# Optimization experiments

Measured on AMD Instinct MI355X. Metric: run time of the kernel, lower is better.

Reference implementation:

```python
import jax, jax.numpy as jnp
import numpy as np

TOPK = 10
MIN_SIM = 0.8
MIN_VOTES = 0.0
REMOVE_INNER_THR = 0.8
NUM_CLASSES = 1000
D, C, N = 256, 256, 500000


def setup_inputs() -> dict:
    key = jax.random.key(0)
    k1, k2, k3, k4, k5 = jax.random.split(key, 5)
    # query descriptors, L2-normalized (cosine similarity, matches min_sim=0.8 semantics)
    q = jax.random.normal(k1, (D, C), dtype=jnp.float32)
    q = q / jnp.linalg.norm(q, axis=1, keepdims=True)
    # database descriptors + integer place_id stored as the last float column
    x = jax.random.normal(k2, (N, C), dtype=jnp.float32)
    x = x / jnp.linalg.norm(x, axis=1, keepdims=True)
    ids = jax.random.randint(k3, (N,), 0, NUM_CLASSES).astype(jnp.float32)
    places_db = jnp.concatenate([x, ids[:, None]], axis=1)  # (N, C+1)
    # valid xyxy boxes in a ~1000px image
    xy = jax.random.uniform(k4, (D, 2), dtype=jnp.float32) * 800.0
    wh = jax.random.uniform(k5, (D, 2), dtype=jnp.float32) * 200.0 + 1.0
    final_boxes = jnp.concatenate([xy, xy + wh], axis=1)  # (D, 4)
    return {"final_boxes": final_boxes, "descriptors": q, "places_db": places_db}


def _remove_overlapping_boxes(boxes, labels, thr):
    # boxes: (D,4) xyxy, labels: (D,) int32
    b = boxes.astype(jnp.float32)
    areas = (b[:, 2] - b[:, 0]) * (b[:, 3] - b[:, 1])  # (D,)
    xi1 = jnp.maximum(b[:, None, 0], b[None, :, 0])
    yi1 = jnp.maximum(b[:, None, 1], b[None, :, 1])
    xi2 = jnp.minimum(b[:, None, 2], b[None, :, 2])
    yi2 = jnp.minimum(b[:, None, 3], b[None, :, 3])
    inter = jnp.clip(xi2 - xi1, 0.0) * jnp.clip(yi2 - yi1, 0.0)  # (D,D)
    area_i = areas[:, None]
    area_j = areas[None, :]
    area_small = jnp.minimum(area_i, area_j)
    overlap = jnp.where(area_small > 0, inter / jnp.where(area_small > 0, area_small, 1.0), 0.0)
    same_lbl = (labels[:, None] == labels[None, :]) & (labels[:, None] >= 0)
    n = boxes.shape[0]
    non_diag = ~jnp.eye(n, dtype=bool)
    mask_pair = same_lbl & (overlap >= thr) & non_diag
    bigger_i = area_i > area_j
    remove_i = jnp.any(mask_pair & bigger_i, axis=1)
    remove_j = jnp.any(mask_pair & ~bigger_i, axis=0)
    remove = remove_i | remove_j
    return jnp.where(remove, jnp.full_like(labels, -1), labels)


def reference(final_boxes, descriptors, places_db):
    X = places_db[:, :-1]                       # (N, C)
    idx = places_db[:, -1].astype(jnp.int32)    # (N,)
    sims = descriptors @ X.T                    # (D, N)
    top_sims, top_idx = jax.lax.top_k(sims, TOPK)  # (D, K)
    top_ids = idx[top_idx]                      # (D, K)
    mask_sim = top_sims >= MIN_SIM              # (D, K)
    one_hot = jax.nn.one_hot(top_ids, NUM_CLASSES, dtype=jnp.float32)  # (D, K, Ncls)
    vote_counts = jnp.sum(one_hot * mask_sim[..., None].astype(jnp.float32), axis=1)  # (D, Ncls)
    majority_counts = jnp.max(vote_counts, axis=1)
    majority_ids = jnp.argmax(vote_counts, axis=1).astype(jnp.int32)
    valid_votes = jnp.sum(mask_sim, axis=1).astype(jnp.float32)
    vote_ratio = jnp.where(valid_votes > 0, majority_counts / jnp.where(valid_votes > 0, valid_votes, 1.0), 0.0)
    valid = (majority_counts > 0) & (vote_ratio >= MIN_VOTES)
    results = jnp.where(valid, majority_ids, jnp.full_like(majority_ids, -1))
    results = _remove_overlapping_boxes(final_boxes, results, REMOVE_INNER_THR)
    match = (top_ids == results[:, None]) & mask_sim
    sim_scores = jnp.max(jnp.where(match, top_sims, jnp.zeros_like(top_sims)), axis=1)  # (D,)
    return (final_boxes, sim_scores, results)
```

## Files before the change

### kernel.cpp

```cpp
#include <hip/hip_runtime.h>
#include <stdint.h>

#define NQ      256
#define NC      256
#define NDB     500000
#define ROWLEN  257
#define MIN_SIM_F 0.8f
#define NMS_THR   0.8f
#define CAP     64
#define TILE    16
#define NTILES  (NDB / TILE)
#define GEMM_GRID 512

typedef __bf16 bf16x8 __attribute__((ext_vector_type(8)));
typedef float  f32x4  __attribute__((ext_vector_type(4)));

union BU { unsigned short u[8]; bf16x8 v; };

__device__ __forceinline__ unsigned short f2bf(float f) {
    uint32_t u = __float_as_uint(f);
    u += 0x7FFFu + ((u >> 16) & 1u);
    return (unsigned short)(u >> 16);
}

__global__ void init_counts(int* cnt) { cnt[threadIdx.x] = 0; }

__global__ __launch_bounds__(256, 2) void gemm_filter(
    const float* __restrict__ q, const float* __restrict__ db,
    int* __restrict__ cnt, float* __restrict__ csim, int* __restrict__ cidx)
{
    __shared__ __align__(16) unsigned short Bs[TILE][264];

    const int tid  = threadIdx.x;
    const int wave = tid >> 6;
    const int lane = tid & 63;
    const int quad = lane >> 4;
    const int l16  = lane & 15;

    bf16x8 a[4][8];
    #pragma unroll
    for (int f = 0; f < 4; ++f) {
        const int m = wave * 64 + f * 16 + l16;
        const float* qrow = q + m * NC;
        #pragma unroll
        for (int s = 0; s < 8; ++s) {
            const int k0 = s * 32 + quad * 8;
            BU u;
            #pragma unroll
            for (int j = 0; j < 8; ++j) u.u[j] = f2bf(qrow[k0 + j]);
            a[f][s] = u.v;
        }
    }

    for (int tile = blockIdx.x; tile < NTILES; tile += gridDim.x) {
        __syncthreads();
        const float* src = db + (size_t)tile * (TILE * ROWLEN);
        for (int g = tid; g < TILE * ROWLEN; g += 256) {
            const int row = g / ROWLEN;
            const int col = g - row * ROWLEN;
            Bs[row][col] = f2bf(src[g]);
        }
        __syncthreads();

        f32x4 zero = {0.f, 0.f, 0.f, 0.f};
        f32x4 acc[4] = {zero, zero, zero, zero};
        #pragma unroll
        for (int s = 0; s < 8; ++s) {
            const bf16x8 b = *(const bf16x8*)&Bs[l16][s * 32 + quad * 8];
            #pragma unroll
            for (int f = 0; f < 4; ++f)
                acc[f] = __builtin_amdgcn_mfma_f32_16x16x32_bf16(a[f][s], b, acc[f], 0, 0, 0);
        }

        float mx = acc[0][0];
        #pragma unroll
        for (int f = 0; f < 4; ++f)
            #pragma unroll
            for (int r = 0; r < 4; ++r) mx = fmaxf(mx, acc[f][r]);
        if (mx >= MIN_SIM_F) {
            const int rowg = tile * TILE + l16;
            #pragma unroll
            for (int f = 0; f < 4; ++f) {
                #pragma unroll
                for (int r = 0; r < 4; ++r) {
                    const float sv = acc[f][r];
                    if (sv >= MIN_SIM_F) {
                        const int qi = wave * 64 + f * 16 + quad * 4 + r;
                        const int pos = atomicAdd(&cnt[qi], 1);
                        if (pos < CAP) {
                            csim[qi * CAP + pos] = sv;
                            cidx[qi * CAP + pos] = rowg;
                        }
                    }
                }
            }
        }
    }
}

__device__ __forceinline__ bool better(float s1, int i1, float s2, int i2) {
    return (s1 > s2) || (s1 == s2 && i1 < i2);
}

__global__ __launch_bounds__(256) void postprocess(
    const float* __restrict__ boxes, const float* __restrict__ db,
    const int* __restrict__ cnt, const float* __restrict__ csim,
    const int* __restrict__ cidx, float* __restrict__ out)
{
    __shared__ int   lab[NQ];
    __shared__ float area_s[NQ];
    __shared__ float bx[NQ][4];

    const int q = threadIdx.x;

    float s10[10]; int i10[10];
    int k = 0;
    int c = cnt[q]; if (c > CAP) c = CAP;
    for (int j = 0; j < c; ++j) {
        const float s = csim[q * CAP + j];
        const int   ix = cidx[q * CAP + j];
        int p;
        if (k < 10) { p = k; ++k; }
        else { if (!better(s, ix, s10[9], i10[9])) continue; p = 9; }
        while (p > 0 && better(s, ix, s10[p - 1], i10[p - 1])) {
            s10[p] = s10[p - 1]; i10[p] = i10[p - 1]; --p;
        }
        s10[p] = s; i10[p] = ix;
    }

    int vid[10];
    for (int j = 0; j < k; ++j) vid[j] = (int)db[(size_t)i10[j] * ROWLEN + (ROWLEN - 1)];
    int best_cnt = 0, best_id = 0x7fffffff;
    for (int j = 0; j < k; ++j) {
        int cj = 0;
        for (int l = 0; l < k; ++l) cj += (vid[l] == vid[j]) ? 1 : 0;
        if (cj > best_cnt || (cj == best_cnt && vid[j] < best_id)) { best_cnt = cj; best_id = vid[j]; }
    }
    const int lq = (best_cnt > 0) ? best_id : -1;
    lab[q] = lq;

    const float x1 = boxes[q * 4 + 0], y1 = boxes[q * 4 + 1];
    const float x2 = boxes[q * 4 + 2], y2 = boxes[q * 4 + 3];
    bx[q][0] = x1; bx[q][1] = y1; bx[q][2] = x2; bx[q][3] = y2;
    const float aq = (x2 - x1) * (y2 - y1);
    area_s[q] = aq;
    __syncthreads();

    bool rem = false;
    if (lq >= 0) {
        for (int p = 0; p < NQ; ++p) {
            if (p == q || lab[p] != lq) continue;
            const float ap = area_s[p];
            if (ap > aq) continue;
            const float xi1 = fmaxf(x1, bx[p][0]);
            const float yi1 = fmaxf(y1, bx[p][1]);
            const float xi2 = fminf(x2, bx[p][2]);
            const float yi2 = fminf(y2, bx[p][3]);
            const float inter = fmaxf(xi2 - xi1, 0.f) * fmaxf(yi2 - yi1, 0.f);
            const float small = fminf(aq, ap);
            const float ov = (small > 0.f) ? inter / small : 0.f;
            if (ov >= NMS_THR) { rem = true; break; }
        }
    }
    const int lq2 = rem ? -1 : lq;

    float score = 0.f;
    if (lq2 >= 0)
        for (int j = 0; j < k; ++j)
            if (vid[j] == lq2) score = fmaxf(score, s10[j]);

    for (int t = q; t < NQ * 4; t += NQ) out[t] = boxes[t];
    out[NQ * 4 + q] = score;
    out[NQ * 5 + q] = (float)lq2;
}

extern "C" void kernel_launch(void* const* d_in, const int* in_sizes, int n_in,
                              void* d_out, int out_size, void* d_ws, size_t ws_size,
                              hipStream_t stream) {
    const float* boxes = (const float*)d_in[0];
    const float* desc  = (const float*)d_in[1];
    const float* db    = (const float*)d_in[2];
    float* out = (float*)d_out;

    int*   cnt  = (int*)d_ws;
    float* csim = (float*)((char*)d_ws + 1024);
    int*   cidx = (int*)((char*)d_ws + 1024 + NQ * CAP * 4);

    init_counts<<<1, 256, 0, stream>>>(cnt);
    gemm_filter<<<GEMM_GRID, 256, 0, stream>>>(desc, db, cnt, csim, cidx);
    postprocess<<<1, 256, 0, stream>>>(boxes, db, cnt, csim, cidx, out);
}
```

Baseline: 690.5 us.

## Double-buffer DB tiles with register prefetch and vectorized float4 loads

The GEMM-filter kernel now uses 512-thread blocks and 32-row tiles, with each wave covering 32 queries and two 16-row B fragments. The next tile is prefetched into registers as float4 loads while the current tile is computed, then converted to bf16 into a second LDS buffer, leaving one barrier per iteration. This targets the memory-bound streaming of the 500k-row database by overlapping global loads with MFMA work and replacing scalar per-element loads that needed an integer division. In exchange it adds register pressure, a more complex index remap for the 257-wide rows, and a launch bound of 4 blocks per CU.

New measurement: 772.8 us. 11.9% more time.

```diff
diff --git a/kernel.cpp b/kernel.cpp
--- a/kernel.cpp
+++ b/kernel.cpp
@@ -8,8 +8,9 @@
 #define MIN_SIM_F 0.8f
 #define NMS_THR   0.8f
 #define CAP     64
-#define TILE    16
+#define TILE    32
 #define NTILES  (NDB / TILE)
+#define BLK     512
 #define GEMM_GRID 512
 
 typedef __bf16 bf16x8 __attribute__((ext_vector_type(8)));
@@ -25,11 +26,11 @@
 
 __global__ void init_counts(int* cnt) { cnt[threadIdx.x] = 0; }
 
-__global__ __launch_bounds__(256, 2) void gemm_filter(
+__global__ __launch_bounds__(BLK, 4) void gemm_filter(
     const float* __restrict__ q, const float* __restrict__ db,
     int* __restrict__ cnt, float* __restrict__ csim, int* __restrict__ cidx)
 {
-    __shared__ __align__(16) unsigned short Bs[TILE][264];
+    __shared__ __align__(16) unsigned short Bs[2][TILE][264];
 
     const int tid  = threadIdx.x;
     const int wave = tid >> 6;
@@ -37,10 +38,10 @@
     const int quad = lane >> 4;
     const int l16  = lane & 15;
 
-    bf16x8 a[4][8];
+    bf16x8 a[2][8];
     #pragma unroll
-    for (int f = 0; f < 4; ++f) {
-        const int m = wave * 64 + f * 16 + l16;
+    for (int f = 0; f < 2; ++f) {
+        const int m = wave * 32 + f * 16 + l16;
         const float* qrow = q + m * NC;
         #pragma unroll
         for (int s = 0; s < 8; ++s) {
@@ -52,49 +53,95 @@
         }
     }
 
-    for (int tile = blockIdx.x; tile < NTILES; tile += gridDim.x) {
-        __syncthreads();
-        const float* src = db + (size_t)tile * (TILE * ROWLEN);
-        for (int g = tid; g < TILE * ROWLEN; g += 256) {
-            const int row = g / ROWLEN;
-            const int col = g - row * ROWLEN;
-            Bs[row][col] = f2bf(src[g]);
-        }
-        __syncthreads();
-
-        f32x4 zero = {0.f, 0.f, 0.f, 0.f};
-        f32x4 acc[4] = {zero, zero, zero, zero};
+    f32x4 r0, r1, r2, r3, rx;
+
+    auto LOAD = [&](int tile) {
+        const f32x4* src = (const f32x4*)(db + (size_t)tile * (TILE * ROWLEN));
+        r0 = src[tid];
+        r1 = src[tid + 512];
+        r2 = src[tid + 1024];
+        r3 = src[tid + 1536];
+        if (tid < 8) rx = src[2048 + tid];
+    };
+
+    auto WRITE = [&](int nb) {
+        unsigned short* dst = &Bs[nb][0][0];
+        #pragma unroll
+        for (int i = 0; i < 5; ++i) {
+            if (i == 4 && tid >= 8) break;
+            const int idx = (i < 4) ? (tid + i * 512) : (2048 + tid);
+            const f32x4 v = (i == 0) ? r0 : (i == 1) ? r1 : (i == 2) ? r2
+                          : (i == 3) ? r3 : rx;
+            const int f   = idx * 4;
+            const int row = f / 257;
+            const int col = f - row * 257;
+            const int base = row * 264 + col;
+            #pragma unroll
+            for (int j = 0; j < 4; ++j) {
+                const int adr = base + j + ((col + j >= 257) ? 7 : 0);
+                dst[adr] = f2bf(v[j]);
+            }
+        }
+    };
+
+    auto COMPUTE = [&](int cb, int tile) {
+        const f32x4 zero = {0.f, 0.f, 0.f, 0.f};
+        f32x4 acc[2][2] = {{zero, zero}, {zero, zero}};
         #pragma unroll
         for (int s = 0; s < 8; ++s) {
-            const bf16x8 b = *(const bf16x8*)&Bs[l16][s * 32 + quad * 8];
-            #pragma unroll
-            for (int f = 0; f < 4; ++f)
-                acc[f] = __builtin_amdgcn_mfma_f32_16x16x32_bf16(a[f][s], b, acc[f], 0, 0, 0);
-        }
-
-        float mx = acc[0][0];
-        #pragma unroll
-        for (int f = 0; f < 4; ++f)
-            #pragma unroll
-            for (int r = 0; r < 4; ++r) mx = fmaxf(mx, acc[f][r]);
+            const int c0 = s * 32 + quad * 8;
+            const bf16x8 b0 = *(const bf16x8*)&Bs[cb][l16][c0];
+            const bf16x8 b1 = *(const bf16x8*)&Bs[cb][16 + l16][c0];
+            acc[0][0] = __builtin_amdgcn_mfma_f32_16x16x32_bf16(a[0][s], b0, acc[0][0], 0, 0, 0);
+            acc[1][0] = __builtin_amdgcn_mfma_f32_16x16x32_bf16(a[1][s], b0, acc[1][0], 0, 0, 0);
+            acc[0][1] = __builtin_amdgcn_mfma_f32_16x16x32_bf16(a[0][s], b1, acc[0][1], 0, 0, 0);
+            acc[1][1] = __builtin_amdgcn_mfma_f32_16x16x32_bf16(a[1][s], b1, acc[1][1], 0, 0, 0);
+        }
+        float mx = acc[0][0][0];
+        #pragma unroll
+        for (int fm = 0; fm < 2; ++fm)
+            #pragma unroll
+            for (int fn = 0; fn < 2; ++fn)
+                #pragma unroll
+                for (int rr = 0; rr < 4; ++rr) mx = fmaxf(mx, acc[fm][fn][rr]);
         if (mx >= MIN_SIM_F) {
-            const int rowg = tile * TILE + l16;
-            #pragma unroll
-            for (int f = 0; f < 4; ++f) {
+            #pragma unroll
+            for (int fm = 0; fm < 2; ++fm) {
                 #pragma unroll
-                for (int r = 0; r < 4; ++r) {
-                    const float sv = acc[f][r];
-                    if (sv >= MIN_SIM_F) {
-                        const int qi = wave * 64 + f * 16 + quad * 4 + r;
-                        const int pos = atomicAdd(&cnt[qi], 1);
-                        if (pos < CAP) {
-                            csim[qi * CAP + pos] = sv;
-                            cidx[qi * CAP + pos] = rowg;
+                for (int fn = 0; fn < 2; ++fn) {
+                    #pragma unroll
+                    for (int rr = 0; rr < 4; ++rr) {
+                        const float sv = acc[fm][fn][rr];
+                        if (sv >= MIN_SIM_F) {
+                            const int qi   = wave * 32 + fm * 16 + quad * 4 + rr;
+                            const int rowg = tile * TILE + fn * 16 + l16;
+                            const int pos = atomicAdd(&cnt[qi], 1);
+                            if (pos < CAP) {
+                                csim[qi * CAP + pos] = sv;
+                                cidx[qi * CAP + pos] = rowg;
+                            }
                         }
                     }
                 }
             }
         }
+    };
+
+    int tile = blockIdx.x;
+    LOAD(tile);
+    WRITE(0);
+    __syncthreads();
+    int buf = 0;
+    for (;;) {
+        const int next = tile + GEMM_GRID;
+        const bool more = (next < NTILES);
+        if (more) LOAD(next);
+        COMPUTE(buf, tile);
+        if (!more) break;
+        WRITE(buf ^ 1);
+        __syncthreads();
+        buf ^= 1;
+        tile = next;
     }
 }
 
@@ -187,6 +234,6 @@
     int*   cidx = (int*)((char*)d_ws + 1024 + NQ * CAP * 4);
 
     init_counts<<<1, 256, 0, stream>>>(cnt);
-    gemm_filter<<<GEMM_GRID, 256, 0, stream>>>(desc, db, cnt, csim, cidx);
+    gemm_filter<<<GEMM_GRID, BLK, 0, stream>>>(desc, db, cnt, csim, cidx);
     postprocess<<<1, 256, 0, stream>>>(boxes, db, cnt, csim, cidx, out);
 }
```
